# Kernel tuning notes

Hardware: AMD Instinct MI355X
Metric: run time of the kernel (lower is better)

Reference implementation:

```python
import jax, jax.numpy as jnp
import numpy as np

N, E, DIN, HID, HEADS = 50000, 1600000, 256, 256, 4
C = (HID // 2) // HEADS  # 32 per-head channels; HEADS*C = HID//2 per direction
NEG_SLOPE = 0.2
BN_EPS = 1e-5


def setup_inputs() -> dict:
    key = jax.random.key(0)
    ks = jax.random.split(key, 16)
    s = lambda k, shp: (jax.random.normal(k, shp, jnp.float32) * 0.05)
    return {
        "x": jax.random.normal(ks[0], (N, DIN), jnp.float32),
        "edge_index": jax.random.randint(ks[1], (2, E), 0, N, jnp.int32),
        # forward-direction GATConv params
        "W_f": s(ks[2], (DIN, HEADS * C)),
        "a_src_f": s(ks[3], (HEADS, C)),
        "a_dst_f": s(ks[4], (HEADS, C)),
        "b_f": jnp.zeros((HEADS * C,), jnp.float32),
        # backward-direction GATConv params
        "W_b": s(ks[5], (DIN, HEADS * C)),
        "a_src_b": s(ks[6], (HEADS, C)),
        "a_dst_b": s(ks[7], (HEADS, C)),
        "b_b": jnp.zeros((HEADS * C,), jnp.float32),
        # fusion linear + batchnorm (eval mode)
        "W_fuse": s(ks[8], (HID, HID)),
        "b_fuse": jnp.zeros((HID,), jnp.float32),
        "gamma": jnp.ones((HID,), jnp.float32),
        "beta": jnp.zeros((HID,), jnp.float32),
        "run_mean": jnp.zeros((HID,), jnp.float32),
        "run_var": jnp.ones((HID,), jnp.float32),
    }


def _gat(x, W, a_src, a_dst, b, src, dst):
    # x: [N, DIN]; src/dst: [E'] (self loops included)
    xl = (x @ W).reshape(N, HEADS, C)               # per-head projected features
    al = jnp.einsum("nhc,hc->nh", xl, a_src)        # [N, H]
    ar = jnp.einsum("nhc,hc->nh", xl, a_dst)        # [N, H]
    e = jax.nn.leaky_relu(al[src] + ar[dst], NEG_SLOPE)  # [E', H]
    # segment softmax over edges sharing the same destination node
    m = jax.ops.segment_max(e, dst, num_segments=N)      # [N, H]
    w = jnp.exp(e - m[dst])
    den = jax.ops.segment_sum(w, dst, num_segments=N)    # [N, H]
    alpha = w / (den[dst] + 1e-16)                       # [E', H]
    msg = xl[src] * alpha[..., None]                     # [E', H, C]
    out = jax.ops.segment_sum(msg, dst, num_segments=N)  # [N, H, C]
    return out.reshape(N, HEADS * C) + b


def reference(x, edge_index, W_f, a_src_f, a_dst_f, b_f, W_b, a_src_b, a_dst_b, b_b,
              W_fuse, b_fuse, gamma, beta, run_mean, run_var):
    loop = jnp.arange(N, dtype=edge_index.dtype)
    src = jnp.concatenate([edge_index[0], loop])  # add self loops (PyG default)
    dst = jnp.concatenate([edge_index[1], loop])
    fwd = _gat(x, W_f, a_src_f, a_dst_f, b_f, src, dst)   # [N, HID//2]
    bwd = _gat(x, W_b, a_src_b, a_dst_b, b_b, dst, src)   # reversed edges
    h = jnp.concatenate([fwd, bwd], axis=1) @ W_fuse + b_fuse  # [N, HID]
    h = (h - run_mean) * jax.lax.rsqrt(run_var + BN_EPS) * gamma + beta
    return jax.nn.relu(h)
```

## Files before the change

kernel.cpp:

```cpp
#include <hip/hip_runtime.h>

#define N_NODES 50000
#define N_EDGES 1600000
#define NEG_SLOPE 0.2f
#define LOG2E 1.44269504f

#define NBUCK 98
#define BSH 9
#define NPB 512
#define CHUNK 6400
#define NBLK 250

typedef __attribute__((ext_vector_type(8))) short short8;
typedef __attribute__((ext_vector_type(4))) float floatx4;

__device__ __forceinline__ unsigned short f2bf(float f) {
  unsigned u = __float_as_uint(f);
  u += 0x7FFFu + ((u >> 16) & 1);
  return (unsigned short)(u >> 16);
}
__device__ __forceinline__ float bflo(unsigned u) { return __uint_as_float(u << 16); }
__device__ __forceinline__ float bfhi(unsigned u) { return __uint_as_float(u & 0xFFFF0000u); }

__global__ __launch_bounds__(256) void k_setup(
    const int* __restrict__ ei, int* __restrict__ blockhist,
    const float* __restrict__ W_f, const float* __restrict__ W_b,
    const float* __restrict__ W_fu,
    unsigned short* __restrict__ Bt1, unsigned short* __restrict__ Bt2,
    const float* __restrict__ x, unsigned short* __restrict__ Xb16)
{
  const int tid = threadIdx.x;
  if (blockIdx.x >= NBLK + 256) {
    const unsigned gid = (unsigned)(blockIdx.x - (NBLK + 256)) * 256u + tid;
    const unsigned row = gid >> 6, c = (gid & 63) * 4;
    float4 v = *(const float4*)(x + (size_t)row * 256 + c);
    *(ushort4*)(Xb16 + (size_t)row * 256 + c) =
        make_ushort4(f2bf(v.x), f2bf(v.y), f2bf(v.z), f2bf(v.w));
    return;
  }
  if (blockIdx.x >= NBLK) {
    const int k = blockIdx.x - NBLK;
    float w1 = (tid < 128) ? W_f[k * 128 + tid] : W_b[k * 128 + (tid - 128)];
    Bt1[(size_t)tid * 256 + k] = f2bf(w1);
    Bt2[(size_t)tid * 256 + k] = f2bf(W_fu[k * 256 + tid]);
    return;
  }
  __shared__ int hist[2 * NBUCK];
  const int blk = blockIdx.x;
  for (int i = tid; i < 2 * NBUCK; i += 256) hist[i] = 0;
  __syncthreads();
  const int e0 = blk * CHUNK;
  for (int e = e0 + tid; e < e0 + CHUNK; e += 256) {
    int s = ei[e];
    int d = ei[N_EDGES + e];
    atomicAdd(&hist[d >> BSH], 1);
    atomicAdd(&hist[NBUCK + (s >> BSH)], 1);
  }
  __syncthreads();
  for (int i = tid; i < 2 * NBUCK; i += 256)
    blockhist[i * NBLK + blk] = hist[i];
}

__global__ __launch_bounds__(256) void k_rowscan(const int* __restrict__ blockhist,
                                                 int* __restrict__ blockoffs, int* __restrict__ bucktotal) {
  const int i = blockIdx.x;
  const int t = threadIdx.x;
  __shared__ int s[256];
  int v = (t < NBLK) ? blockhist[i * NBLK + t] : 0;
  s[t] = v;
  __syncthreads();
  for (int off = 1; off < 256; off <<= 1) {
    int u = (t >= off) ? s[t - off] : 0;
    __syncthreads();
    s[t] += u;
    __syncthreads();
  }
  if (t < NBLK) blockoffs[i * NBLK + t] = s[t] - v;
  if (t == 255) bucktotal[i] = s[255];
}

__global__ __launch_bounds__(256) void k_buckscan(const int* __restrict__ bucktotal,
                                                  int* __restrict__ buckbase, int* rpf, int* rpb) {
  __shared__ int s[256];
  const int t = threadIdx.x;
  int v = (t < 2 * NBUCK) ? bucktotal[t] : 0;
  s[t] = v;
  __syncthreads();
  for (int off = 1; off < 256; off <<= 1) {
    int u = (t >= off) ? s[t - off] : 0;
    __syncthreads();
    s[t] += u;
    __syncthreads();
  }
  if (t < 2 * NBUCK) {
    const int dir = (t >= NBUCK) ? 1 : 0;
    const int b = t - dir * NBUCK;
    const int sub = dir ? s[NBUCK - 1] : 0;
    buckbase[dir * (NBUCK + 1) + b] = s[t] - v - sub;
    if (b == NBUCK - 1) buckbase[dir * (NBUCK + 1) + NBUCK] = s[t] - sub;
  }
  if (t == 0) { rpf[N_NODES] = N_EDGES + N_NODES; rpb[N_NODES] = N_EDGES + N_NODES; }
}

__global__ __launch_bounds__(256) void k_stage(const int* __restrict__ ei,
                                               const int* __restrict__ blockoffs,
                                               const int* __restrict__ buckbase,
                                               unsigned* __restrict__ staging) {
  __shared__ int cur[2 * NBUCK];
  const int blk = blockIdx.x, tid = threadIdx.x;
  for (int i = tid; i < 2 * NBUCK; i += 256) {
    int dir = (i >= NBUCK) ? 1 : 0;
    int b = i - dir * NBUCK;
    cur[i] = blockoffs[i * NBLK + blk] + buckbase[dir * (NBUCK + 1) + b];
  }
  __syncthreads();
  unsigned* st0 = staging;
  unsigned* st1 = staging + N_EDGES;
  const int e0 = blk * CHUNK;
  for (int e = e0 + tid; e < e0 + CHUNK; e += 256) {
    int s = ei[e];
    int d = ei[N_EDGES + e];
    int p = atomicAdd(&cur[d >> BSH], 1);
    st0[p] = ((unsigned)(d & (NPB - 1)) << 16) | (unsigned)s;
    int q = atomicAdd(&cur[NBUCK + (s >> BSH)], 1);
    st1[q] = ((unsigned)(s & (NPB - 1)) << 16) | (unsigned)d;
  }
}

__global__ __launch_bounds__(512) void k_bin(const unsigned* __restrict__ staging,
                                             const int* __restrict__ buckbase,
                                             int* __restrict__ rpf, int* __restrict__ rpb,
                                             int* __restrict__ adjf, int* __restrict__ adjb) {
  const int b = blockIdx.x, dir = blockIdx.y, tid = threadIdx.x;
  const int node0 = b << BSH;
  const int nn = min(NPB, N_NODES - node0);
  const unsigned* st = staging + (size_t)dir * N_EDGES;
  int* rp  = dir ? rpb : rpf;
  int* adj = dir ? adjb : adjf;
  const int beg = buckbase[dir * (NBUCK + 1) + b];
  const int end = buckbase[dir * (NBUCK + 1) + b + 1];

  __shared__ int cnt[NPB];
  __shared__ int wpart[8];
  cnt[tid] = 0;
  __syncthreads();
  for (int jj = beg + tid; jj < end; jj += 512)
    atomicAdd(&cnt[st[jj] >> 16], 1);
  __syncthreads();
  const int deg1 = (tid < nn) ? cnt[tid] + 1 : 0;
  int v = deg1;
  const int wl = tid & 63;
#pragma unroll
  for (int off = 1; off < 64; off <<= 1) {
    int u = __shfl_up(v, off, 64);
    if (wl >= off) v += u;
  }
  if (wl == 63) wpart[tid >> 6] = v;
  __syncthreads();
  int pre = 0;
#pragma unroll
  for (int w = 0; w < 7; ++w)
    if (w < (tid >> 6)) pre += wpart[w];
  const int excl = v + pre - deg1;
  if (tid < nn) {
    int r = beg + node0 + excl;
    rp[node0 + tid] = r;
    adj[r] = node0 + tid;
    cnt[tid] = r + 1;
  }
  __syncthreads();
  for (int jj = beg + tid; jj < end; jj += 512) {
    unsigned rec = st[jj];
    int p = atomicAdd(&cnt[rec >> 16], 1);
    adj[p] = (int)(rec & 0xFFFFu);
  }
}

#define LDA 40

__global__ __launch_bounds__(256) void k_mm(
    const unsigned short* __restrict__ A, int M,
    const unsigned short* __restrict__ Bt,
    unsigned short* __restrict__ D0, unsigned short* __restrict__ D1,
    float* __restrict__ Df, int mode,
    const float* __restrict__ bias, const float* __restrict__ gamma,
    const float* __restrict__ beta, const float* __restrict__ mean,
    const float* __restrict__ var)
{
  __shared__ __align__(16) unsigned short As[128 * LDA];
  __shared__ __align__(16) unsigned short Bs[128 * LDA];
  const int tid = threadIdx.x;
  const int m0 = blockIdx.x * 128, col0 = blockIdx.y * 128;
  const int wave = tid >> 6, lane = tid & 63;
  const int wm = wave >> 1, wn = wave & 1;
  const int lm = lane & 15, quad = lane >> 4;

  floatx4 acc[4][4];
#pragma unroll
  for (int i = 0; i < 4; ++i)
#pragma unroll
    for (int j = 0; j < 4; ++j) acc[i][j] = (floatx4){0.f, 0.f, 0.f, 0.f};

  for (int it = 0; it < 8; ++it) {
    const int kk0 = it * 32;
    __syncthreads();
#pragma unroll
    for (int q = 0; q < 2; ++q) {
      int idx = q * 256 + tid;
      int r = idx >> 2, c8 = (idx & 3) * 8;
      ulonglong2 z; z.x = 0; z.y = 0;
      if (m0 + r < M) z = *(const ulonglong2*)(A + (size_t)(m0 + r) * 256 + kk0 + c8);
      *(ulonglong2*)&As[r * LDA + c8] = z;
    }
#pragma unroll
    for (int q = 0; q < 2; ++q) {
      int idx = q * 256 + tid;
      int nc = idx >> 2, c8 = (idx & 3) * 8;
      ulonglong2 z = *(const ulonglong2*)(Bt + (size_t)(col0 + nc) * 256 + kk0 + c8);
      *(ulonglong2*)&Bs[nc * LDA + c8] = z;
    }
    __syncthreads();
    short8 a[4], b[4];
#pragma unroll
    for (int i = 0; i < 4; ++i)
      a[i] = *(const short8*)&As[(wm * 64 + i * 16 + lm) * LDA + quad * 8];
#pragma unroll
    for (int j = 0; j < 4; ++j)
      b[j] = *(const short8*)&Bs[(wn * 64 + j * 16 + lm) * LDA + quad * 8];
#pragma unroll
    for (int i = 0; i < 4; ++i)
#pragma unroll
      for (int j = 0; j < 4; ++j)
        acc[i][j] = __builtin_amdgcn_mfma_f32_16x16x32_bf16(a[i], b[j], acc[i][j], 0, 0, 0);
  }

  if (mode == 0) {
    unsigned short* C = (col0 >= 128) ? D1 : D0;
#pragma unroll
    for (int i = 0; i < 4; ++i) {
#pragma unroll
      for (int j = 0; j < 4; ++j) {
        int lc = (wn * 64 + j * 16 + lm);
#pragma unroll
        for (int reg = 0; reg < 4; ++reg) {
          int gr = m0 + wm * 64 + i * 16 + quad * 4 + reg;
          if (gr < M) C[(size_t)gr * 128 + lc] = f2bf(acc[i][j][reg]);
        }
      }
    }
  } else {
#pragma unroll
    for (int j = 0; j < 4; ++j) {
      int gc = col0 + wn * 64 + j * 16 + lm;
      float bi = bias[gc], mu = mean[gc], iv = rsqrtf(var[gc] + 1e-5f);
      float ga = gamma[gc], be = beta[gc];
#pragma unroll
      for (int i = 0; i < 4; ++i) {
#pragma unroll
        for (int reg = 0; reg < 4; ++reg) {
          int gr = m0 + wm * 64 + i * 16 + quad * 4 + reg;
          if (gr < M) {
            float v = acc[i][j][reg] + bi;
            v = (v - mu) * iv * ga + be;
            Df[(size_t)gr * 256 + gc] = fmaxf(v, 0.f);
          }
        }
      }
    }
  }
}

__global__ __launch_bounds__(256) void k_scores(
    const unsigned short* __restrict__ Xf, const unsigned short* __restrict__ Xb,
    const float* __restrict__ asf, const float* __restrict__ adf,
    const float* __restrict__ asb, const float* __restrict__ adb,
    float* __restrict__ ALf, float* __restrict__ ARf,
    float* __restrict__ ALb, float* __restrict__ ARb)
{
  const int wave = threadIdx.x >> 6, lane = threadIdx.x & 63;
  const int n = blockIdx.x * 4 + wave;
  const int hh = lane >> 5;
  const int c = lane & 31;
  float v0 = bflo((unsigned)Xf[(size_t)n * 128 + lane]);
  float v1 = bflo((unsigned)Xf[(size_t)n * 128 + 64 + lane]);
  float v2 = bflo((unsigned)Xb[(size_t)n * 128 + lane]);
  float v3 = bflo((unsigned)Xb[(size_t)n * 128 + 64 + lane]);
  float s0 = v0 * asf[hh * 32 + c],       d0 = v0 * adf[hh * 32 + c];
  float s1 = v1 * asf[(2 + hh) * 32 + c], d1 = v1 * adf[(2 + hh) * 32 + c];
  float s2 = v2 * asb[hh * 32 + c],       d2 = v2 * adb[hh * 32 + c];
  float s3 = v3 * asb[(2 + hh) * 32 + c], d3 = v3 * adb[(2 + hh) * 32 + c];
#pragma unroll
  for (int off = 16; off > 0; off >>= 1) {
    s0 += __shfl_xor(s0, off, 32); d0 += __shfl_xor(d0, off, 32);
    s1 += __shfl_xor(s1, off, 32); d1 += __shfl_xor(d1, off, 32);
    s2 += __shfl_xor(s2, off, 32); d2 += __shfl_xor(d2, off, 32);
    s3 += __shfl_xor(s3, off, 32); d3 += __shfl_xor(d3, off, 32);
  }
  if (c == 0) {
    ALf[n * 4 + hh] = s0 * LOG2E;     ARf[n * 4 + hh] = d0 * LOG2E;
    ALf[n * 4 + 2 + hh] = s1 * LOG2E; ARf[n * 4 + 2 + hh] = d1 * LOG2E;
    ALb[n * 4 + hh] = s2 * LOG2E;     ARb[n * 4 + hh] = d2 * LOG2E;
    ALb[n * 4 + 2 + hh] = s3 * LOG2E; ARb[n * 4 + 2 + hh] = d3 * LOG2E;
  }
}

__global__ __launch_bounds__(256) void k_agg(
    const uint2* __restrict__ Xf, const uint2* __restrict__ Xb,
    const int* __restrict__ rpf, const int* __restrict__ adjf,
    const int* __restrict__ rpb, const int* __restrict__ adjb,
    const float* __restrict__ ALf, const float* __restrict__ ARf,
    const float* __restrict__ ALb, const float* __restrict__ ARb,
    const float* __restrict__ bf, const float* __restrict__ bb,
    unsigned* __restrict__ H16)
{
  const int dir = blockIdx.y;
  const int wave = threadIdx.x >> 6;
  const int n = blockIdx.x * 4 + wave;
  const uint2* X = dir ? Xb : Xf;
  const int* rp  = dir ? rpb : rpf;
  const int* adj = dir ? adjb : adjf;
  const float* AL = dir ? ALb : ALf;
  const float* AR = dir ? ARb : ARf;
  const float* bias = dir ? bb : bf;
  const int lane = threadIdx.x & 63;
  const int sub = lane >> 5;
  const unsigned t = (unsigned)(lane & 31);
  const unsigned h = t >> 3;
  const float arn = AR[((unsigned)n << 2) | h];
  const int beg = rp[n], end = rp[n + 1];
  const int cntE = end - beg;
  const int full = cntE >> 1;
  float a0 = 0.f, a1 = 0.f, a2 = 0.f, a3 = 0.f, den = 0.f;
  const int* ap = adj + beg + sub;
#pragma unroll 4
  for (int it = 0; it < full; ++it, ap += 2) {
    int nb = *ap;
    float al = AL[((unsigned)nb << 2) | h];
    uint2 u = X[((unsigned)nb << 5) | t];
    float s = al + arn;
    float e = fmaxf(s, s * NEG_SLOPE);
    float w = exp2f(e);
    den += w;
    a0 = fmaf(w, bflo(u.x), a0);
    a1 = fmaf(w, bfhi(u.x), a1);
    a2 = fmaf(w, bflo(u.y), a2);
    a3 = fmaf(w, bfhi(u.y), a3);
  }
  if (cntE & 1) {
    int nb = adj[end - 1];
    float al = AL[((unsigned)nb << 2) | h];
    uint2 u = X[((unsigned)nb << 5) | t];
    float s = al + arn;
    float e = fmaxf(s, s * NEG_SLOPE);
    float w = exp2f(e);
    w = (sub == 0) ? w : 0.f;
    den += w;
    a0 = fmaf(w, bflo(u.x), a0);
    a1 = fmaf(w, bfhi(u.x), a1);
    a2 = fmaf(w, bflo(u.y), a2);
    a3 = fmaf(w, bfhi(u.y), a3);
  }
  a0 += __shfl_xor(a0, 32); a1 += __shfl_xor(a1, 32);
  a2 += __shfl_xor(a2, 32); a3 += __shfl_xor(a3, 32);
  den += __shfl_xor(den, 32);
  if (sub == 0) {
    float inv = 1.f / (den + 1e-16f);
    float4 bv = *(const float4*)(bias + 4 * t);
    float v0 = a0 * inv + bv.x, v1 = a1 * inv + bv.y;
    float v2 = a2 * inv + bv.z, v3 = a3 * inv + bv.w;
    uint2 hw;
    hw.x = ((unsigned)f2bf(v1) << 16) | f2bf(v0);
    hw.y = ((unsigned)f2bf(v3) << 16) | f2bf(v2);
    unsigned base = (unsigned)n * 128u + (unsigned)dir * 64u + 2u * t;
    *(uint2*)(H16 + base) = hw;
  }
}


extern "C" void kernel_launch(void* const* d_in, const int* in_sizes, int n_in,
                              void* d_out, int out_size, void* d_ws, size_t ws_size,
                              hipStream_t stream) {
  const float* x    = (const float*)d_in[0];
  const int*   ei   = (const int*)d_in[1];
  const float* W_f  = (const float*)d_in[2];
  const float* asf  = (const float*)d_in[3];
  const float* adf  = (const float*)d_in[4];
  const float* b_f  = (const float*)d_in[5];
  const float* W_b  = (const float*)d_in[6];
  const float* asb  = (const float*)d_in[7];
  const float* adb  = (const float*)d_in[8];
  const float* b_b  = (const float*)d_in[9];
  const float* W_fu = (const float*)d_in[10];
  const float* b_fu = (const float*)d_in[11];
  const float* gam  = (const float*)d_in[12];
  const float* bet  = (const float*)d_in[13];
  const float* mean = (const float*)d_in[14];
  const float* var  = (const float*)d_in[15];
  float* out = (float*)d_out;

  char* base = (char*)d_ws;
  size_t off = 0;
  auto alloc = [&](size_t bytes) {
    void* p = base + off;
    off = (off + bytes + 255) & ~(size_t)255;
    return p;
  };
  unsigned short* Xb16 = (unsigned short*)alloc((size_t)N_NODES * 256 * 2);
  unsigned* H16        = (unsigned*)Xb16;
  unsigned short* Xf   = (unsigned short*)alloc((size_t)N_NODES * 128 * 2);
  unsigned short* Xb   = (unsigned short*)alloc((size_t)N_NODES * 128 * 2);
  unsigned short* Bt1  = (unsigned short*)alloc((size_t)256 * 256 * 2);
  unsigned short* Bt2  = (unsigned short*)alloc((size_t)256 * 256 * 2);
  float* ALf  = (float*)alloc((size_t)N_NODES * 4 * 4);
  float* ARf  = (float*)alloc((size_t)N_NODES * 4 * 4);
  float* ALb  = (float*)alloc((size_t)N_NODES * 4 * 4);
  float* ARb  = (float*)alloc((size_t)N_NODES * 4 * 4);
  int* rpf    = (int*)alloc((size_t)(N_NODES + 1) * 4);
  int* rpb    = (int*)alloc((size_t)(N_NODES + 1) * 4);
  int* adjf   = (int*)alloc((size_t)(N_EDGES + N_NODES) * 4);
  int* adjb   = (int*)alloc((size_t)(N_EDGES + N_NODES) * 4);
  int* blockhist = (int*)alloc((size_t)2 * NBUCK * NBLK * 4);
  int* blockoffs = (int*)alloc((size_t)2 * NBUCK * NBLK * 4);
  int* bucktotal = (int*)alloc((size_t)2 * NBUCK * 4);
  int* buckbase  = (int*)alloc((size_t)2 * (NBUCK + 1) * 4);
  unsigned* staging = (unsigned*)alloc((size_t)2 * N_EDGES * 4);
  (void)ws_size; (void)in_sizes; (void)n_in; (void)out_size;

  const int XB = (N_NODES * 64) / 256;
  k_setup<<<NBLK + 256 + XB, 256, 0, stream>>>(ei, blockhist, W_f, W_b, W_fu,
                                               Bt1, Bt2, x, Xb16);
  k_rowscan<<<2 * NBUCK, 256, 0, stream>>>(blockhist, blockoffs, bucktotal);
  k_buckscan<<<1, 256, 0, stream>>>(bucktotal, buckbase, rpf, rpb);
  k_stage<<<NBLK, 256, 0, stream>>>(ei, blockoffs, buckbase, staging);
  k_bin<<<dim3(NBUCK, 2), 512, 0, stream>>>(staging, buckbase, rpf, rpb, adjf, adjb);

  const int MB = (N_NODES + 127) / 128;
  k_mm<<<dim3(MB, 2), 256, 0, stream>>>(Xb16, N_NODES, Bt1, Xf, Xb, nullptr, 0,
                                        nullptr, nullptr, nullptr, nullptr, nullptr);
  k_scores<<<N_NODES / 4, 256, 0, stream>>>(Xf, Xb, asf, adf, asb, adb,
                                            ALf, ARf, ALb, ARb);
  k_agg<<<dim3(N_NODES / 4, 2), 256, 0, stream>>>((const uint2*)Xf, (const uint2*)Xb,
                                                  rpf, adjf, rpb, adjb,
                                                  ALf, ARf, ALb, ARb, b_f, b_b, H16);
  k_mm<<<dim3(MB, 2), 256, 0, stream>>>((const unsigned short*)H16, N_NODES, Bt2,
                                        nullptr, nullptr, out, 1,
                                        b_fu, gam, bet, mean, var);
}
```

Measured before the change: 383.1 us.

## Co-schedule graph build with GEMM/scores and widen aggregation gathers to uint4

The edge staging kernel and the first projection GEMM now run as one launch, with blocks split by index and shared memory held in a union. Likewise, CSR binning and the attention-score computation share one launch. Both pairings let independent work overlap and remove launch gaps. The aggregation kernel now processes four edges per wave with 16 lanes each, loading uint4 (8 bf16) per lane, and uses the hardware exp2 builtin. The risk is that register pressure and shared-memory size in the fused kernels may cut occupancy, and the wider gather changes per-lane reduction cost.

```diff
diff --git a/kernel.cpp b/kernel.cpp
--- a/kernel.cpp
+++ b/kernel.cpp
@@ -21,6 +21,13 @@
 }
 __device__ __forceinline__ float bflo(unsigned u) { return __uint_as_float(u << 16); }
 __device__ __forceinline__ float bfhi(unsigned u) { return __uint_as_float(u & 0xFFFF0000u); }
+__device__ __forceinline__ float fexp2(float x) {
+#if __has_builtin(__builtin_amdgcn_exp2f)
+  return __builtin_amdgcn_exp2f(x);
+#else
+  return exp2f(x);
+#endif
+}
 
 __global__ __launch_bounds__(256) void k_setup(
     const int* __restrict__ ei, int* __restrict__ blockhist,
@@ -102,95 +109,19 @@
   if (t == 0) { rpf[N_NODES] = N_EDGES + N_NODES; rpb[N_NODES] = N_EDGES + N_NODES; }
 }
 
-__global__ __launch_bounds__(256) void k_stage(const int* __restrict__ ei,
-                                               const int* __restrict__ blockoffs,
-                                               const int* __restrict__ buckbase,
-                                               unsigned* __restrict__ staging) {
-  __shared__ int cur[2 * NBUCK];
-  const int blk = blockIdx.x, tid = threadIdx.x;
-  for (int i = tid; i < 2 * NBUCK; i += 256) {
-    int dir = (i >= NBUCK) ? 1 : 0;
-    int b = i - dir * NBUCK;
-    cur[i] = blockoffs[i * NBLK + blk] + buckbase[dir * (NBUCK + 1) + b];
-  }
-  __syncthreads();
-  unsigned* st0 = staging;
-  unsigned* st1 = staging + N_EDGES;
-  const int e0 = blk * CHUNK;
-  for (int e = e0 + tid; e < e0 + CHUNK; e += 256) {
-    int s = ei[e];
-    int d = ei[N_EDGES + e];
-    int p = atomicAdd(&cur[d >> BSH], 1);
-    st0[p] = ((unsigned)(d & (NPB - 1)) << 16) | (unsigned)s;
-    int q = atomicAdd(&cur[NBUCK + (s >> BSH)], 1);
-    st1[q] = ((unsigned)(s & (NPB - 1)) << 16) | (unsigned)d;
-  }
-}
-
-__global__ __launch_bounds__(512) void k_bin(const unsigned* __restrict__ staging,
-                                             const int* __restrict__ buckbase,
-                                             int* __restrict__ rpf, int* __restrict__ rpb,
-                                             int* __restrict__ adjf, int* __restrict__ adjb) {
-  const int b = blockIdx.x, dir = blockIdx.y, tid = threadIdx.x;
-  const int node0 = b << BSH;
-  const int nn = min(NPB, N_NODES - node0);
-  const unsigned* st = staging + (size_t)dir * N_EDGES;
-  int* rp  = dir ? rpb : rpf;
-  int* adj = dir ? adjb : adjf;
-  const int beg = buckbase[dir * (NBUCK + 1) + b];
-  const int end = buckbase[dir * (NBUCK + 1) + b + 1];
-
-  __shared__ int cnt[NPB];
-  __shared__ int wpart[8];
-  cnt[tid] = 0;
-  __syncthreads();
-  for (int jj = beg + tid; jj < end; jj += 512)
-    atomicAdd(&cnt[st[jj] >> 16], 1);
-  __syncthreads();
-  const int deg1 = (tid < nn) ? cnt[tid] + 1 : 0;
-  int v = deg1;
-  const int wl = tid & 63;
-#pragma unroll
-  for (int off = 1; off < 64; off <<= 1) {
-    int u = __shfl_up(v, off, 64);
-    if (wl >= off) v += u;
-  }
-  if (wl == 63) wpart[tid >> 6] = v;
-  __syncthreads();
-  int pre = 0;
-#pragma unroll
-  for (int w = 0; w < 7; ++w)
-    if (w < (tid >> 6)) pre += wpart[w];
-  const int excl = v + pre - deg1;
-  if (tid < nn) {
-    int r = beg + node0 + excl;
-    rp[node0 + tid] = r;
-    adj[r] = node0 + tid;
-    cnt[tid] = r + 1;
-  }
-  __syncthreads();
-  for (int jj = beg + tid; jj < end; jj += 512) {
-    unsigned rec = st[jj];
-    int p = atomicAdd(&cnt[rec >> 16], 1);
-    adj[p] = (int)(rec & 0xFFFFu);
-  }
-}
-
 #define LDA 40
 
-__global__ __launch_bounds__(256) void k_mm(
+__device__ __forceinline__ void mm_body(
     const unsigned short* __restrict__ A, int M,
     const unsigned short* __restrict__ Bt,
     unsigned short* __restrict__ D0, unsigned short* __restrict__ D1,
     float* __restrict__ Df, int mode,
     const float* __restrict__ bias, const float* __restrict__ gamma,
     const float* __restrict__ beta, const float* __restrict__ mean,
-    const float* __restrict__ var)
-{
-  __shared__ __align__(16) unsigned short As[128 * LDA];
-  __shared__ __align__(16) unsigned short Bs[128 * LDA];
+    const float* __restrict__ var,
+    int m0, int col0, unsigned short* As, unsigned short* Bs)
+{
   const int tid = threadIdx.x;
-  const int m0 = blockIdx.x * 128, col0 = blockIdx.y * 128;
   const int wave = tid >> 6, lane = tid & 63;
   const int wm = wave >> 1, wn = wave & 1;
   const int lm = lane & 15, quad = lane >> 4;
@@ -270,15 +201,104 @@
   }
 }
 
-__global__ __launch_bounds__(256) void k_scores(
+__global__ __launch_bounds__(256) void k_stage_mm(
+    const int* __restrict__ ei, const int* __restrict__ blockoffs,
+    const int* __restrict__ buckbase, unsigned* __restrict__ staging,
+    const unsigned short* __restrict__ Xb16, const unsigned short* __restrict__ Bt1,
+    unsigned short* __restrict__ Xf, unsigned short* __restrict__ Xb)
+{
+  __shared__ union {
+    int cur[2 * NBUCK];
+    struct { unsigned short As[128 * LDA]; unsigned short Bs[128 * LDA]; } mm;
+  } sm;
+  const int tid = threadIdx.x;
+  if (blockIdx.x < NBLK) {
+    const int blk = blockIdx.x;
+    for (int i = tid; i < 2 * NBUCK; i += 256) {
+      int dir = (i >= NBUCK) ? 1 : 0;
+      int b = i - dir * NBUCK;
+      sm.cur[i] = blockoffs[i * NBLK + blk] + buckbase[dir * (NBUCK + 1) + b];
+    }
+    __syncthreads();
+    unsigned* st0 = staging;
+    unsigned* st1 = staging + N_EDGES;
+    const int e0 = blk * CHUNK;
+    for (int e = e0 + tid; e < e0 + CHUNK; e += 256) {
+      int s = ei[e];
+      int d = ei[N_EDGES + e];
+      int p = atomicAdd(&sm.cur[d >> BSH], 1);
+      st0[p] = ((unsigned)(d & (NPB - 1)) << 16) | (unsigned)s;
+      int q = atomicAdd(&sm.cur[NBUCK + (s >> BSH)], 1);
+      st1[q] = ((unsigned)(s & (NPB - 1)) << 16) | (unsigned)d;
+    }
+    return;
+  }
+  const int bid = blockIdx.x - NBLK;
+  mm_body(Xb16, N_NODES, Bt1, Xf, Xb, nullptr, 0,
+          nullptr, nullptr, nullptr, nullptr, nullptr,
+          (bid >> 1) * 128, (bid & 1) * 128, sm.mm.As, sm.mm.Bs);
+}
+
+__global__ __launch_bounds__(512) void k_bin_scores(
+    const unsigned* __restrict__ staging, const int* __restrict__ buckbase,
+    int* __restrict__ rpf, int* __restrict__ rpb,
+    int* __restrict__ adjf, int* __restrict__ adjb,
     const unsigned short* __restrict__ Xf, const unsigned short* __restrict__ Xb,
     const float* __restrict__ asf, const float* __restrict__ adf,
     const float* __restrict__ asb, const float* __restrict__ adb,
     float* __restrict__ ALf, float* __restrict__ ARf,
     float* __restrict__ ALb, float* __restrict__ ARb)
 {
-  const int wave = threadIdx.x >> 6, lane = threadIdx.x & 63;
-  const int n = blockIdx.x * 4 + wave;
+  const int tid = threadIdx.x;
+  if (blockIdx.x < 2 * NBUCK) {
+    const int dir = (blockIdx.x >= NBUCK) ? 1 : 0;
+    const int b = blockIdx.x - dir * NBUCK;
+    const int node0 = b << BSH;
+    const int nn = min(NPB, N_NODES - node0);
+    const unsigned* st = staging + (size_t)dir * N_EDGES;
+    int* rp  = dir ? rpb : rpf;
+    int* adj = dir ? adjb : adjf;
+    const int beg = buckbase[dir * (NBUCK + 1) + b];
+    const int end = buckbase[dir * (NBUCK + 1) + b + 1];
+
+    __shared__ int cnt[NPB];
+    __shared__ int wpart[8];
+    cnt[tid] = 0;
+    __syncthreads();
+    for (int jj = beg + tid; jj < end; jj += 512)
+      atomicAdd(&cnt[st[jj] >> 16], 1);
+    __syncthreads();
+    const int deg1 = (tid < nn) ? cnt[tid] + 1 : 0;
+    int v = deg1;
+    const int wl = tid & 63;
+#pragma unroll
+    for (int off = 1; off < 64; off <<= 1) {
+      int u = __shfl_up(v, off, 64);
+      if (wl >= off) v += u;
+    }
+    if (wl == 63) wpart[tid >> 6] = v;
+    __syncthreads();
+    int pre = 0;
+#pragma unroll
+    for (int w = 0; w < 7; ++w)
+      if (w < (tid >> 6)) pre += wpart[w];
+    const int excl = v + pre - deg1;
+    if (tid < nn) {
+      int r = beg + node0 + excl;
+      rp[node0 + tid] = r;
+      adj[r] = node0 + tid;
+      cnt[tid] = r + 1;
+    }
+    __syncthreads();
+    for (int jj = beg + tid; jj < end; jj += 512) {
+      unsigned rec = st[jj];
+      int p = atomicAdd(&cnt[rec >> 16], 1);
+      adj[p] = (int)(rec & 0xFFFFu);
+    }
+    return;
+  }
+  const int wave = tid >> 6, lane = tid & 63;
+  const int n = (blockIdx.x - 2 * NBUCK) * 8 + wave;
   const int hh = lane >> 5;
   const int c = lane & 31;
   float v0 = bflo((unsigned)Xf[(size_t)n * 128 + lane]);
@@ -305,7 +325,7 @@
 }
 
 __global__ __launch_bounds__(256) void k_agg(
-    const uint2* __restrict__ Xf, const uint2* __restrict__ Xb,
+    const uint4* __restrict__ Xf, const uint4* __restrict__ Xb,
     const int* __restrict__ rpf, const int* __restrict__ adjf,
     const int* __restrict__ rpb, const int* __restrict__ adjb,
     const float* __restrict__ ALf, const float* __restrict__ ARf,
@@ -316,64 +336,91 @@
   const int dir = blockIdx.y;
   const int wave = threadIdx.x >> 6;
   const int n = blockIdx.x * 4 + wave;
-  const uint2* X = dir ? Xb : Xf;
+  const uint4* X = dir ? Xb : Xf;
   const int* rp  = dir ? rpb : rpf;
   const int* adj = dir ? adjb : adjf;
   const float* AL = dir ? ALb : ALf;
   const float* AR = dir ? ARb : ARf;
   const float* bias = dir ? bb : bf;
   const int lane = threadIdx.x & 63;
-  const int sub = lane >> 5;
-  const unsigned t = (unsigned)(lane & 31);
-  const unsigned h = t >> 3;
+  const int sg = lane >> 4;
+  const unsigned l = (unsigned)(lane & 15);
+  const unsigned h = l >> 2;
   const float arn = AR[((unsigned)n << 2) | h];
   const int beg = rp[n], end = rp[n + 1];
   const int cntE = end - beg;
-  const int full = cntE >> 1;
-  float a0 = 0.f, a1 = 0.f, a2 = 0.f, a3 = 0.f, den = 0.f;
-  const int* ap = adj + beg + sub;
+  const int full = cntE >> 2;
+  float a0 = 0.f, a1 = 0.f, a2 = 0.f, a3 = 0.f;
+  float a4 = 0.f, a5 = 0.f, a6 = 0.f, a7 = 0.f, den = 0.f;
+  const int* ap = adj + beg + sg;
 #pragma unroll 4
-  for (int it = 0; it < full; ++it, ap += 2) {
+  for (int it = 0; it < full; ++it, ap += 4) {
     int nb = *ap;
     float al = AL[((unsigned)nb << 2) | h];
-    uint2 u = X[((unsigned)nb << 5) | t];
+    uint4 u = X[((unsigned)nb << 4) | l];
     float s = al + arn;
     float e = fmaxf(s, s * NEG_SLOPE);
-    float w = exp2f(e);
+    float w = fexp2(e);
     den += w;
-    a0 = fmaf(w, bflo(u.x), a0);
-    a1 = fmaf(w, bfhi(u.x), a1);
-    a2 = fmaf(w, bflo(u.y), a2);
-    a3 = fmaf(w, bfhi(u.y), a3);
-  }
-  if (cntE & 1) {
-    int nb = adj[end - 1];
+    a0 = fmaf(w, bflo(u.x), a0); a1 = fmaf(w, bfhi(u.x), a1);
+    a2 = fmaf(w, bflo(u.y), a2); a3 = fmaf(w, bfhi(u.y), a3);
+    a4 = fmaf(w, bflo(u.z), a4); a5 = fmaf(w, bfhi(u.z), a5);
+    a6 = fmaf(w, bflo(u.w), a6); a7 = fmaf(w, bfhi(u.w), a7);
+  }
+  const int rem = cntE & 3;
+  if (rem) {
+    int j = beg + 4 * full + sg;
+    int jj = (sg < rem) ? j : beg;
+    int nb = adj[jj];
     float al = AL[((unsigned)nb << 2) | h];
-    uint2 u = X[((unsigned)nb << 5) | t];
+    uint4 u = X[((unsigned)nb << 4) | l];
     float s = al + arn;
     float e = fmaxf(s, s * NEG_SLOPE);
-    float w = exp2f(e);
-    w = (sub == 0) ? w : 0.f;
+    float w = fexp2(e);
+    w = (sg < rem) ? w : 0.f;
     den += w;
-    a0 = fmaf(w, bflo(u.x), a0);
-    a1 = fmaf(w, bfhi(u.x), a1);
-    a2 = fmaf(w, bflo(u.y), a2);
-    a3 = fmaf(w, bfhi(u.y), a3);
-  }
-  a0 += __shfl_xor(a0, 32); a1 += __shfl_xor(a1, 32);
-  a2 += __shfl_xor(a2, 32); a3 += __shfl_xor(a3, 32);
-  den += __shfl_xor(den, 32);
-  if (sub == 0) {
+    a0 = fmaf(w, bflo(u.x), a0); a1 = fmaf(w, bfhi(u.x), a1);
+    a2 = fmaf(w, bflo(u.y), a2); a3 = fmaf(w, bfhi(u.y), a3);
+    a4 = fmaf(w, bflo(u.z), a4); a5 = fmaf(w, bfhi(u.z), a5);
+    a6 = fmaf(w, bflo(u.w), a6); a7 = fmaf(w, bfhi(u.w), a7);
+  }
+#pragma unroll
+  for (int off = 16; off <= 32; off <<= 1) {
+    a0 += __shfl_xor(a0, off); a1 += __shfl_xor(a1, off);
+    a2 += __shfl_xor(a2, off); a3 += __shfl_xor(a3, off);
+    a4 += __shfl_xor(a4, off); a5 += __shfl_xor(a5, off);
+    a6 += __shfl_xor(a6, off); a7 += __shfl_xor(a7, off);
+    den += __shfl_xor(den, off);
+  }
+  if (lane < 16) {
     float inv = 1.f / (den + 1e-16f);
-    float4 bv = *(const float4*)(bias + 4 * t);
-    float v0 = a0 * inv + bv.x, v1 = a1 * inv + bv.y;
-    float v2 = a2 * inv + bv.z, v3 = a3 * inv + bv.w;
-    uint2 hw;
+    float4 b0 = *(const float4*)(bias + 8 * l);
+    float4 b1 = *(const float4*)(bias + 8 * l + 4);
+    float v0 = a0 * inv + b0.x, v1 = a1 * inv + b0.y;
+    float v2 = a2 * inv + b0.z, v3 = a3 * inv + b0.w;
+    float v4 = a4 * inv + b1.x, v5 = a5 * inv + b1.y;
+    float v6 = a6 * inv + b1.z, v7 = a7 * inv + b1.w;
+    uint4 hw;
     hw.x = ((unsigned)f2bf(v1) << 16) | f2bf(v0);
     hw.y = ((unsigned)f2bf(v3) << 16) | f2bf(v2);
-    unsigned base = (unsigned)n * 128u + (unsigned)dir * 64u + 2u * t;
-    *(uint2*)(H16 + base) = hw;
-  }
+    hw.z = ((unsigned)f2bf(v5) << 16) | f2bf(v4);
+    hw.w = ((unsigned)f2bf(v7) << 16) | f2bf(v6);
+    *(uint4*)(H16 + (unsigned)n * 128u + (unsigned)dir * 64u + 4u * l) = hw;
+  }
+}
+
+__global__ __launch_bounds__(256) void k_mm2(
+    const unsigned short* __restrict__ A, const unsigned short* __restrict__ Bt,
+    float* __restrict__ Df,
+    const float* __restrict__ bias, const float* __restrict__ gamma,
+    const float* __restrict__ beta, const float* __restrict__ mean,
+    const float* __restrict__ var)
+{
+  __shared__ __align__(16) unsigned short As[128 * LDA];
+  __shared__ __align__(16) unsigned short Bs[128 * LDA];
+  mm_body(A, N_NODES, Bt, nullptr, nullptr, Df, 1,
+          bias, gamma, beta, mean, var,
+          blockIdx.x * 128, blockIdx.y * 128, As, Bs);
 }
 
 
@@ -427,22 +474,20 @@
   (void)ws_size; (void)in_sizes; (void)n_in; (void)out_size;
 
   const int XB = (N_NODES * 64) / 256;
+  const int MB = (N_NODES + 127) / 128;
+
   k_setup<<<NBLK + 256 + XB, 256, 0, stream>>>(ei, blockhist, W_f, W_b, W_fu,
                                                Bt1, Bt2, x, Xb16);
   k_rowscan<<<2 * NBUCK, 256, 0, stream>>>(blockhist, blockoffs, bucktotal);
   k_buckscan<<<1, 256, 0, stream>>>(bucktotal, buckbase, rpf, rpb);
-  k_stage<<<NBLK, 256, 0, stream>>>(ei, blockoffs, buckbase, staging);
-  k_bin<<<dim3(NBUCK, 2), 512, 0, stream>>>(staging, buckbase, rpf, rpb, adjf, adjb);
-
-  const int MB = (N_NODES + 127) / 128;
-  k_mm<<<dim3(MB, 2), 256, 0, stream>>>(Xb16, N_NODES, Bt1, Xf, Xb, nullptr, 0,
-                                        nullptr, nullptr, nullptr, nullptr, nullptr);
-  k_scores<<<N_NODES / 4, 256, 0, stream>>>(Xf, Xb, asf, adf, asb, adb,
-                                            ALf, ARf, ALb, ARb);
-  k_agg<<<dim3(N_NODES / 4, 2), 256, 0, stream>>>((const uint2*)Xf, (const uint2*)Xb,
+  k_stage_mm<<<NBLK + MB * 2, 256, 0, stream>>>(ei, blockoffs, buckbase, staging,
+                                                Xb16, Bt1, Xf, Xb);
+  k_bin_scores<<<2 * NBUCK + N_NODES / 8, 512, 0, stream>>>(
+      staging, buckbase, rpf, rpb, adjf, adjb,
+      Xf, Xb, asf, adf, asb, adb, ALf, ARf, ALb, ARb);
+  k_agg<<<dim3(N_NODES / 4, 2), 256, 0, stream>>>((const uint4*)Xf, (const uint4*)Xb,
                                                   rpf, adjf, rpb, adjb,
                                                   ALf, ARf, ALb, ARb, b_f, b_b, H16);
-  k_mm<<<dim3(MB, 2), 256, 0, stream>>>((const unsigned short*)H16, N_NODES, Bt2,
-                                        nullptr, nullptr, out, 1,
-                                        b_fu, gam, bet, mean, var);
-}
+  k_mm2<<<dim3(MB, 2), 256, 0, stream>>>((const unsigned short*)H16, Bt2, out,
+                                         b_fu, gam, bet, mean, var);
+}
```

After: 350.7 us. 1.09x faster.
